# Optimization experiments

Hardware: AMD Instinct MI355X
Metric: run time of the kernel (lower is better)

Reference implementation:

```python
import jax, jax.numpy as jnp
import numpy as np
import math

B, S, HID = 2, 2048, 1024
NH = 16
HD = HID // NH          # 64
VD = HD // 2            # 32 value dim
TD = HD - VD            # 32 type dim
EPS = 1e-6


def setup_inputs() -> dict:
    key = jax.random.key(0)
    ks = jax.random.split(key, 12)
    std = 1.0 / math.sqrt(HID)
    xav = math.sqrt(6.0 / (TD + TD))
    return {
        "x": jax.random.normal(ks[0], (B, S, HID), dtype=jnp.float32),
        "q_w": jax.random.uniform(ks[1], (HID, HID), jnp.float32, -std, std),
        "q_b": jax.random.uniform(ks[2], (HID,), jnp.float32, -std, std),
        "k_w": jax.random.uniform(ks[3], (HID, HID), jnp.float32, -std, std),
        "k_b": jax.random.uniform(ks[4], (HID,), jnp.float32, -std, std),
        "v_w": jax.random.uniform(ks[5], (HID, HID), jnp.float32, -std, std),
        "v_b": jax.random.uniform(ks[6], (HID,), jnp.float32, -std, std),
        "out_w": jax.random.uniform(ks[7], (HID, HID), jnp.float32, -std, std),
        "out_b": jax.random.uniform(ks[8], (HID,), jnp.float32, -std, std),
        "type_bilinear": jax.random.uniform(ks[9], (NH, TD, TD), jnp.float32, -xav, xav),
        "type_bias": jnp.full((NH,), 2.0, dtype=jnp.float32),
        "mask": jnp.ones((B, S), dtype=jnp.int32),
    }


def reference(x, q_w, q_b, k_w, k_b, v_w, v_b, out_w, out_b, type_bilinear, type_bias, mask):
    # projections: [B,S,HID] -> [B,NH,S,HD]
    def proj(w, b):
        y = jnp.einsum("bsi,io->bso", x, w) + b
        return y.reshape(B, S, NH, HD).transpose(0, 2, 1, 3)

    q = proj(q_w, q_b)
    k = proj(k_w, k_b)
    v = proj(v_w, v_b)

    q_val, q_type = q[..., :VD], q[..., VD:]
    k_val, k_type = k[..., :VD], k[..., VD:]

    # standard value score: [B,NH,S,S]
    val_scores = jnp.einsum("bhqd,bhkd->bhqk", q_val, k_val) / math.sqrt(VD)

    # per-head bilinear type score: q_type @ W_h @ k_type^T + bias_h
    qt = jnp.einsum("bhqd,hde->bhqe", q_type, type_bilinear)
    type_scores = jnp.einsum("bhqe,bhke->bhqk", qt, k_type) + type_bias[None, :, None, None]
    type_unif = jax.nn.sigmoid(type_scores)

    scores = val_scores + jnp.log(type_unif + EPS)

    # mask: [B,S] -> broadcast over heads and query dim (keys masked)
    m = (mask[:, None, None, :] != 0)
    scores = jnp.where(m, scores, -jnp.inf)

    attn = jax.nn.softmax(scores, axis=-1)
    out = jnp.einsum("bhqk,bhkd->bhqd", attn, v)          # [B,NH,S,HD]
    out = out.transpose(0, 2, 1, 3).reshape(B, S, HID)
    return jnp.einsum("bsi,io->bso", out, out_w) + out_b
```

## Files before the change

kernel.cpp:

```cpp
#include <hip/hip_runtime.h>
#include <hip/hip_bf16.h>
#include <math.h>

typedef __attribute__((ext_vector_type(8))) short bf16x8;
typedef __attribute__((ext_vector_type(4))) short bf16x4;
typedef __attribute__((ext_vector_type(4))) float f32x4;
typedef __attribute__((ext_vector_type(4))) int   i32x4;

#define NHh 16
#define Sq  2048
#define HIDq 1024
#define HDq 64
#define LOG2E 1.4426950408889634f

#if __has_builtin(__builtin_amdgcn_exp2f)
#define EXP2F(x) __builtin_amdgcn_exp2f(x)
#else
#define EXP2F(x) exp2f(x)
#endif
#if __has_builtin(__builtin_amdgcn_rcpf)
#define RCPF(x) __builtin_amdgcn_rcpf(x)
#else
#define RCPF(x) (1.0f/(x))
#endif

#if __has_builtin(__builtin_amdgcn_mfma_f32_16x16x16bf16_1k)
__device__ __forceinline__ f32x4 MFMA16(bf16x4 a, bf16x4 b, f32x4 c){
  return __builtin_amdgcn_mfma_f32_16x16x16bf16_1k(a, b, c, 0, 0, 0);
}
#else
__device__ __forceinline__ f32x4 MFMA16(bf16x4 a, bf16x4 b, f32x4 c){
  asm volatile("v_mfma_f32_16x16x16_bf16 %0, %1, %2, %0\n\ts_nop 7\n\ts_nop 7"
               : "+v"(c) : "v"(a), "v"(b));
  return c;
}
#endif

__device__ __forceinline__ unsigned short f2bf(float f){
  union { float f; unsigned u; } v; v.f = f;
  unsigned r = v.u + 0x7fffu + ((v.u >> 16) & 1u);
  return (unsigned short)(r >> 16);
}
__device__ __forceinline__ float bf2f(unsigned short s){
  union { unsigned u; float f; } v; v.u = ((unsigned)s) << 16;
  return v.f;
}
__device__ __forceinline__ unsigned pk2bf(float lo, float hi){
  union { __hip_bfloat162 h; unsigned u; } w;
  w.h = __float22bfloat162_rn(make_float2(lo, hi));
  return w.u;
}

__device__ __forceinline__ void gload_lds16(const unsigned short* g, unsigned short* l){
  __builtin_amdgcn_global_load_lds(
      (const __attribute__((address_space(1))) unsigned int*)g,
      (__attribute__((address_space(3))) unsigned int*)l, 16, 0, 0);
}

__global__ __launch_bounds__(256) void prep(const float* __restrict__ x,
                                            unsigned short* __restrict__ xbf,
                                            const int* __restrict__ mask,
                                            unsigned short* __restrict__ Mbf,
                                            const float* __restrict__ w0, const float* __restrict__ w1,
                                            const float* __restrict__ w2, const float* __restrict__ w3,
                                            unsigned short* __restrict__ wT){
  int bid = blockIdx.x;
  int t = threadIdx.x;
  if (bid < 2048){
    int i = bid*256 + t;
    const f32x4* p = (const f32x4*)(x + (size_t)i*8);
    f32x4 a = p[0], b = p[1];
    union { unsigned short us[8]; i32x4 v; } o;
    #pragma unroll
    for (int j=0;j<4;j++){ o.us[j] = f2bf(a[j]); o.us[4+j] = f2bf(b[j]); }
    *(i32x4*)(xbf + (size_t)i*8) = o.v;
  } else if (bid < 2050){
    int base = (bid - 2048)*2048 + t*8;
    #pragma unroll
    for (int j=0;j<8;j++) Mbf[base+j] = mask[base+j] ? (unsigned short)0x3F80 : (unsigned short)0;
  } else {
    __shared__ float tile[32][33];
    int bid2 = bid - 2050;
    int z = bid2 >> 10, rem = bid2 & 1023;
    int bx = rem & 31, by = rem >> 5;
    const float* w = (z==0)?w0:(z==1)?w1:(z==2)?w2:w3;
    unsigned short* dst = wT + (size_t)z*HIDq*HIDq;
    int tx = t & 31, ty = t >> 5;
    int n0 = bx*32, k0 = by*32;
    #pragma unroll
    for (int i=ty;i<32;i+=8) tile[i][tx] = w[(size_t)(k0+i)*HIDq + n0+tx];
    __syncthreads();
    #pragma unroll
    for (int i=ty;i<32;i+=8) dst[(size_t)(n0+i)*HIDq + k0+tx] = f2bf(tile[tx][i]);
  }
}

__device__ __forceinline__ void gemm_core_gl(const unsigned short* __restrict__ Ag,
                                             const unsigned short* __restrict__ Bg,
                                             unsigned short* As, unsigned short* Bs,
                                             int t, int wv, int lane, int wr, int wc, int lr, int g,
                                             f32x4 acc[4][4]){
  for (int k0=0; k0<HIDq; k0+=64){
    __syncthreads();
    #pragma unroll
    for (int j=0;j<4;j++){
      int flat = (j*4+wv)*64 + lane;
      int row = flat>>3, c = flat&7;
      int srcc = (c ^ (row&7))*8;
      gload_lds16(Ag + (size_t)row*HIDq + k0 + srcc, &As[flat*8]);
      gload_lds16(Bg + (size_t)row*HIDq + k0 + srcc, &Bs[flat*8]);
    }
    __syncthreads();
    #pragma unroll
    for (int ks=0; ks<2; ks++){
      bf16x8 af[4], bfv[4];
      #pragma unroll
      for (int m=0;m<4;m++){
        int rr = wr + m*16 + lr;
        af[m]  = *(bf16x8*)&As[rr*64 + (((ks*4+g) ^ (rr&7))*8)];
      }
      #pragma unroll
      for (int n=0;n<4;n++){
        int rr = wc + n*16 + lr;
        bfv[n] = *(bf16x8*)&Bs[rr*64 + (((ks*4+g) ^ (rr&7))*8)];
      }
      #pragma unroll
      for (int n=0;n<4;n++)
        #pragma unroll
        for (int m=0;m<4;m++)
          acc[n][m] = __builtin_amdgcn_mfma_f32_16x16x32_bf16(bfv[n], af[m], acc[n][m], 0,0,0);
    }
  }
}

__global__ __launch_bounds__(256) void gemm_qkv(const unsigned short* __restrict__ xbf,
    const unsigned short* __restrict__ wT,
    const float* __restrict__ q_b, const float* __restrict__ k_b, const float* __restrict__ v_b,
    const int* __restrict__ mask,
    unsigned short* __restrict__ Qeff, unsigned short* __restrict__ Keff,
    unsigned short* __restrict__ Vt){
  __shared__ unsigned short As[128*64];
  __shared__ unsigned short Bs[128*64];
  const int t = threadIdx.x;
  const int wv = t>>6, lane = t&63, g = lane>>4, lr = lane&15;
  const int wr = (wv>>1)*64, wc = (wv&1)*64;
  f32x4 acc[4][4] = {};
  const int bid = blockIdx.x;
  const int xcd = bid & 7, idx = bid >> 3;
  const int xb = (idx % 3)*8 + xcd;
  const int yb = idx / 3;
  const float VS = 0.25501335f;

  if (xb < 16){
    const int row0 = yb*128, col0 = xb*128;
    gemm_core_gl(xbf + (size_t)row0*HIDq, wT + (size_t)col0*HIDq, As, Bs, t, wv, lane, wr, wc, lr, g, acc);
    #pragma unroll
    for (int n=0;n<4;n++){
      #pragma unroll
      for (int m=0;m<4;m++){
        int row = row0 + wr + m*16 + lr;
        int b_ = row>>11, ss = row&2047;
        int colb = col0 + wc + n*16 + g*4;
        int seg = colb>>10, cw = colb&1023;
        int hh = cw>>6, d = cw&63;
        const float* bp = seg ? k_b : q_b;
        f32x4 bb = *(const f32x4*)&bp[cw];
        float sc = seg ? 1.0f : (d < 32 ? VS : -LOG2E);
        unsigned short* E = seg ? Keff : Qeff;
        float v0 = (acc[n][m][0]+bb[0])*sc, v1 = (acc[n][m][1]+bb[1])*sc;
        float v2 = (acc[n][m][2]+bb[2])*sc, v3 = (acc[n][m][3]+bb[3])*sc;
        union { unsigned u[2]; unsigned long long ll; } W;
        W.u[0] = pk2bf(v0,v1); W.u[1] = pk2bf(v2,v3);
        *(unsigned long long*)&E[(((size_t)b_*NHh+hh)*Sq+ss)*HDq + d] = W.ll;
      }
    }
  } else {
    const int row0 = (xb-16)*128, col0 = yb*128;
    gemm_core_gl(wT + (size_t)2*HIDq*HIDq + (size_t)row0*HIDq, xbf + (size_t)col0*HIDq,
                 As, Bs, t, wv, lane, wr, wc, lr, g, acc);
    #pragma unroll
    for (int n=0;n<4;n++){
      #pragma unroll
      for (int m=0;m<4;m++){
        int chan = row0 + wr + m*16 + lr;
        int hh = chan>>6, d = chan&63;
        float bv = v_b[chan];
        int colb = col0 + wc + n*16 + g*4;
        int b_ = colb>>11, ss = colb&2047;
        i32x4 mk = *(const i32x4*)&mask[(size_t)b_*Sq + ss];
        float m0 = mk[0]?1.f:0.f, m1 = mk[1]?1.f:0.f, m2 = mk[2]?1.f:0.f, m3 = mk[3]?1.f:0.f;
        union { unsigned u[2]; unsigned long long ll; } W;
        W.u[0] = pk2bf((acc[n][m][0]+bv)*m0, (acc[n][m][1]+bv)*m1);
        W.u[1] = pk2bf((acc[n][m][2]+bv)*m2, (acc[n][m][3]+bv)*m3);
        *(unsigned long long*)&Vt[(((size_t)b_*NHh+hh)*HDq + d)*Sq + ss] = W.ll;
      }
    }
  }
}

__global__ __launch_bounds__(256) void gemm_out(const unsigned short* __restrict__ A,
                                                const unsigned short* __restrict__ Bt,
                                                const float* __restrict__ bias,
                                                float* __restrict__ C){
  __shared__ unsigned short As[128*64];
  __shared__ unsigned short Bs[64*64];
  const int t = threadIdx.x;
  const int wv = t>>6, lane = t&63, g = lane>>4, lr = lane&15;
  const int wr = (wv>>1)*64, wc = (wv&1)*32;
  const int row0 = blockIdx.y*128, col0 = blockIdx.x*64;
  f32x4 acc[2][4] = {};
  for (int k0=0; k0<HIDq; k0+=64){
    __syncthreads();
    #pragma unroll
    for (int j=0;j<4;j++){
      int flat = t + j*256;
      int row = flat>>3, c = flat&7;
      int srcc = (c ^ (row&7))*8;
      gload_lds16(A + (size_t)(row0+row)*HIDq + k0 + srcc, &As[flat*8]);
    }
    #pragma unroll
    for (int j=0;j<2;j++){
      int flat = t + j*256;
      int row = flat>>3, c = flat&7;
      int srcc = (c ^ (row&7))*8;
      gload_lds16(Bt + (size_t)(col0+row)*HIDq + k0 + srcc, &Bs[flat*8]);
    }
    __syncthreads();
    #pragma unroll
    for (int ks=0; ks<2; ks++){
      bf16x8 af[4], bfv[2];
      #pragma unroll
      for (int m=0;m<4;m++){
        int rr = wr + m*16 + lr;
        af[m]  = *(bf16x8*)&As[rr*64 + (((ks*4+g) ^ (rr&7))*8)];
      }
      #pragma unroll
      for (int n=0;n<2;n++){
        int rr = wc + n*16 + lr;
        bfv[n] = *(bf16x8*)&Bs[rr*64 + (((ks*4+g) ^ (rr&7))*8)];
      }
      #pragma unroll
      for (int n=0;n<2;n++)
        #pragma unroll
        for (int m=0;m<4;m++)
          acc[n][m] = __builtin_amdgcn_mfma_f32_16x16x32_bf16(bfv[n], af[m], acc[n][m], 0,0,0);
    }
  }
  #pragma unroll
  for (int n=0;n<2;n++){
    #pragma unroll
    for (int m=0;m<4;m++){
      int row = row0 + wr + m*16 + lr;
      int colb = col0 + wc + n*16 + g*4;
      f32x4 bb = *(const f32x4*)&bias[colb];
      f32x4 o = acc[n][m] + bb;
      *(f32x4*)&C[(size_t)row*HIDq + colb] = o;
    }
  }
}

__global__ __launch_bounds__(256,4) void attn_kernel(
    const unsigned short* __restrict__ Qe, const unsigned short* __restrict__ Ke,
    const unsigned short* __restrict__ Vt, const float* __restrict__ Tb,
    const float* __restrict__ tbias, const unsigned short* __restrict__ Mbf,
    unsigned short* __restrict__ Obuf)
{
  __shared__ __align__(16) unsigned char smem[40960];
  unsigned short* Kb0 = (unsigned short*)smem;
  unsigned short* Kb1 = (unsigned short*)(smem + 8192);
  unsigned short* Kb2 = (unsigned short*)(smem + 16384);
  unsigned short* Vb0 = (unsigned short*)(smem + 24576);
  unsigned short* Vb1 = (unsigned short*)(smem + 32768);
  float* qls = (float*)smem;
  unsigned short* qtls = Vb1;

  const int t = threadIdx.x;
  const int dd = blockIdx.x;
  const int slot = dd>>3, xcd = dd&7;
  const int x = slot & 31;
  const int bh = ((slot>>5)<<3) | xcd;
  const int h = bh & 15, b = bh >> 4;
  const int q0 = x*64;
  const int wv = t>>6, lane = t&63, g = lane>>4, lr = lane&15;

  const unsigned short* Qb  = Qe + (((size_t)b*NHh+h)*Sq + q0)*HDq;
  const unsigned short* Kb  = Ke + ((size_t)b*NHh+h)*(size_t)Sq*HDq;
  const unsigned short* Vtb = Vt + ((size_t)b*NHh+h)*(size_t)HDq*Sq;
  const unsigned short* Mbfb = Mbf + (size_t)b*Sq;

  {
    int row = t>>2, c8 = (t&3)*8;
    bf16x8 v = *(const bf16x8*)(Qb + (size_t)row*HDq + 32 + c8);
    #pragma unroll
    for (int j=0;j<8;j++) qls[row*33 + c8 + j] = bf2f((unsigned short)v[j]);
  }
  __syncthreads();
  {
    int row = t&63, e0 = (t>>6)*8;
    const float* Th = Tb + (size_t)h*1024;
    float a[8] = {};
    #pragma unroll 4
    for (int d=0; d<32; d++){
      float qd = qls[row*33 + d];
      const f32x4* tp = (const f32x4*)(Th + d*32 + e0);
      f32x4 t0 = tp[0], t1 = tp[1];
      a[0]+=qd*t0[0]; a[1]+=qd*t0[1]; a[2]+=qd*t0[2]; a[3]+=qd*t0[3];
      a[4]+=qd*t1[0]; a[5]+=qd*t1[1]; a[6]+=qd*t1[2]; a[7]+=qd*t1[3];
    }
    __syncthreads();
    union { unsigned u[2]; unsigned long long ll; } W0, W1;
    W0.u[0]=pk2bf(a[0],a[1]); W0.u[1]=pk2bf(a[2],a[3]);
    W1.u[0]=pk2bf(a[4],a[5]); W1.u[1]=pk2bf(a[6],a[7]);
    *(unsigned long long*)&qtls[row*40 + e0]     = W0.ll;
    *(unsigned long long*)&qtls[row*40 + e0 + 4] = W1.ll;
  }
  bf16x8 qvf = *(const bf16x8*)(Qb + (size_t)(wv*16+lr)*HDq + g*8);
  __syncthreads();
  bf16x8 qtn = *(const bf16x8*)&qtls[(wv*16+lr)*40 + g*8];
  __syncthreads();

  #pragma unroll
  for (int i=0;i<2;i++){
    int c = t + i*256;
    int kr = c>>3, kc = c&7;
    gload_lds16(Kb + (size_t)kr*HDq + ((kc ^ (kr&7))*8), Kb0 + c*8);
    int vd = c>>3, vc = c&7;
    gload_lds16(Vtb + (size_t)vd*Sq + ((vc ^ (vd&7))*8), Vb0 + c*8);
    gload_lds16(Kb + (size_t)(64+kr)*HDq + ((kc ^ (kr&7))*8), Kb1 + c*8);
  }
  __syncthreads();

  const float tbn = -tbias[h]*LOG2E;
  const f32x4 tbc = {tbn,tbn,tbn,tbn};
  const f32x4 zf = {0.f,0.f,0.f,0.f};
  f32x4 oT[4] = {};
  f32x4 lsum = {0.f,0.f,0.f,0.f};

  auto phase = [&](const unsigned short* Kc, const unsigned short* Vc, int key0,
                   bool stK, int keyK, unsigned short* Kn,
                   bool stV, int keyV, unsigned short* Vn, bool vm8){
    if (stK){
      #pragma unroll
      for (int i=0;i<2;i++){
        int c = t + i*256;
        int kr = c>>3, kc = c&7;
        gload_lds16(Kb + (size_t)(keyK+kr)*HDq + ((kc ^ (kr&7))*8), Kn + c*8);
      }
    }
    if (stV){
      #pragma unroll
      for (int i=0;i<2;i++){
        int c = t + i*256;
        int vd = c>>3, vc = c&7;
        gload_lds16(Vtb + (size_t)vd*Sq + keyV + ((vc ^ (vd&7))*8), Vn + c*8);
      }
    }
    if (vm8) asm volatile("s_waitcnt vmcnt(8)" ::: "memory");
    else     asm volatile("s_waitcnt vmcnt(4)" ::: "memory");
    __builtin_amdgcn_sched_barrier(0);
    __builtin_amdgcn_s_barrier();

    f32x4 sv[4], st[4];
    __builtin_amdgcn_s_setprio(1);
    #pragma unroll
    for (int ks=0; ks<4; ks++){
      const unsigned short* kb = Kc + (ks*16+lr)*64;
      bf16x8 kf0 = *(const bf16x8*)(kb + (((g  ) ^ (lr&7))*8));
      bf16x8 kf1 = *(const bf16x8*)(kb + (((4+g) ^ (lr&7))*8));
      sv[ks] = __builtin_amdgcn_mfma_f32_16x16x32_bf16(kf0, qvf, zf, 0,0,0);
      st[ks] = __builtin_amdgcn_mfma_f32_16x16x32_bf16(kf1, qtn, tbc, 0,0,0);
    }
    __builtin_amdgcn_s_setprio(0);
    bf16x4 pa[4];
    #pragma unroll
    for (int ks=0; ks<4; ks++){
      float p0 = EXP2F(sv[ks][0]) * RCPF(1.f + EXP2F(st[ks][0]));
      float p1 = EXP2F(sv[ks][1]) * RCPF(1.f + EXP2F(st[ks][1]));
      float p2 = EXP2F(sv[ks][2]) * RCPF(1.f + EXP2F(st[ks][2]));
      float p3 = EXP2F(sv[ks][3]) * RCPF(1.f + EXP2F(st[ks][3]));
      union { unsigned u[2]; bf16x4 v; } P_;
      P_.u[0] = pk2bf(p0,p1); P_.u[1] = pk2bf(p2,p3);
      pa[ks] = P_.v;
    }
    #pragma unroll
    for (int ks=0; ks<4; ks++){
      bf16x4 mfr = *(const bf16x4*)(Mbfb + key0 + ks*16 + g*4);
      __builtin_amdgcn_s_setprio(1);
      lsum = MFMA16(pa[ks], mfr, lsum);
      #pragma unroll
      for (int db=0; db<4; db++){
        bf16x4 vf = *(const bf16x4*)(Vc + (db*16+lr)*64 + (((2*ks + (g>>1)) ^ (lr&7))*8 + 4*(g&1)));
        oT[db] = MFMA16(pa[ks], vf, oT[db]);
      }
      __builtin_amdgcn_s_setprio(0);
    }
    __builtin_amdgcn_s_barrier();
  };

  for (int j=0; j<5; j++){
    int kt = j*384;
    phase(Kb0, Vb0, kt,      true, kt+128, Kb2,  true, kt+64,  Vb1, true);
    phase(Kb1, Vb1, kt+64,   true, kt+192, Kb0,  true, kt+128, Vb0, true);
    phase(Kb2, Vb0, kt+128,  true, kt+256, Kb1,  true, kt+192, Vb1, true);
    phase(Kb0, Vb1, kt+192,  true, kt+320, Kb2,  true, kt+256, Vb0, true);
    phase(Kb1, Vb0, kt+256,  true, kt+384, Kb0,  true, kt+320, Vb1, true);
    phase(Kb2, Vb1, kt+320,  (kt+448 < Sq), kt+448, Kb1,  true, kt+384, Vb0, true);
  }
  phase(Kb0, Vb0, 1920,  false, 0, Kb0,  true, 1984, Vb1, false);
  phase(Kb1, Vb1, 1984,  false, 0, Kb0,  false, 0, Vb0,  false);

  float linv[4];
  #pragma unroll
  for (int r=0;r<4;r++) linv[r] = (lsum[r] > 0.f) ? RCPF(lsum[r]) : 0.f;
  unsigned short* Ob = Obuf + ((size_t)b*Sq + (q0 + wv*16 + g*4))*HIDq + h*HDq + lr;
  #pragma unroll
  for (int db=0; db<4; db++){
    #pragma unroll
    for (int r=0;r<4;r++)
      Ob[(size_t)r*HIDq + db*16] = f2bf(oT[db][r]*linv[r]);
  }
}

extern "C" void kernel_launch(void* const* d_in, const int* in_sizes, int n_in,
                              void* d_out, int out_size, void* d_ws, size_t ws_size,
                              hipStream_t stream) {
  const float* x     = (const float*)d_in[0];
  const float* q_w   = (const float*)d_in[1];
  const float* q_b   = (const float*)d_in[2];
  const float* k_w   = (const float*)d_in[3];
  const float* k_b   = (const float*)d_in[4];
  const float* v_w   = (const float*)d_in[5];
  const float* v_b   = (const float*)d_in[6];
  const float* out_w = (const float*)d_in[7];
  const float* out_b = (const float*)d_in[8];
  const float* Tb    = (const float*)d_in[9];
  const float* tbias = (const float*)d_in[10];
  const int*   mask  = (const int*)d_in[11];

  const size_t MROWS = 4096;
  unsigned short* xbf  = (unsigned short*)d_ws;
  unsigned short* wT   = xbf  + MROWS*HIDq;
  unsigned short* Qeff = wT   + (size_t)4*HIDq*HIDq;
  unsigned short* Keff = Qeff + MROWS*HIDq;
  unsigned short* Vt   = Keff + MROWS*HIDq;
  unsigned short* Obuf = Vt   + MROWS*HIDq;
  unsigned short* Mbf  = Obuf + MROWS*HIDq;

  prep<<<dim3(6146), dim3(256), 0, stream>>>(x, xbf, mask, Mbf, q_w, k_w, v_w, out_w, wT);

  gemm_qkv<<<dim3(768), dim3(256), 0, stream>>>(xbf, wT, q_b, k_b, v_b, mask, Qeff, Keff, Vt);

  attn_kernel<<<dim3(1024), dim3(256), 0, stream>>>(Qeff, Keff, Vt, Tb, tbias, Mbf, Obuf);

  gemm_out<<<dim3(16,32), dim3(256), 0, stream>>>(Obuf, wT + (size_t)3*HIDq*HIDq, out_b, (float*)d_out);
}
```

Before: 149.0 us.

## Fold per-head type bilinear matrix into Q projection weights and bias

A new small kernel multiplies the type half of each head's Q weight columns and bias by that head's bilinear matrix. It overwrites the transposed bf16 Q weights and writes an effective Q bias. The QKV GEMM therefore emits q_type already multiplied by W_h, so the attention kernel drops its per-block prologue (LDS staging, a 32x32 matmul per row, extra barriers) and loads the type fragment straight from global memory. The cost is an extra launch of a 16-block kernel that runs serially after prep and may take a noticeable share of the runtime. Rounding also changes slightly because the folded product is rounded to bf16 in the weights rather than computed per activation.

```diff
diff --git a/kernel.cpp b/kernel.cpp
--- a/kernel.cpp
+++ b/kernel.cpp
@@ -95,6 +95,44 @@
   }
 }
 
+__global__ __launch_bounds__(256) void fold_T(const float* __restrict__ q_w,
+                                              const float* __restrict__ q_b,
+                                              const float* __restrict__ Tb,
+                                              unsigned short* __restrict__ wTq,
+                                              float* __restrict__ qb_eff){
+  __shared__ float Ts[32][33];
+  const int h = blockIdx.x;
+  const int t = threadIdx.x;
+  if (t < 128){
+    int d = t>>2, e0 = (t&3)*8;
+    #pragma unroll
+    for (int j=0;j<8;j++) Ts[d][e0+j] = Tb[h*1024 + d*32 + e0 + j];
+  }
+  __syncthreads();
+  const int col0 = h*64 + 32;
+  if (t < 32){
+    float a = 0.f;
+    #pragma unroll 8
+    for (int d=0; d<32; d++) a += q_b[col0+d]*Ts[d][t];
+    qb_eff[col0 + t] = a;
+  } else if (t < 64){
+    qb_eff[h*64 + (t-32)] = q_b[h*64 + (t-32)];
+  }
+  for (int k = t; k < HIDq; k += 256){
+    float qr[32];
+    const float* src = q_w + (size_t)k*HIDq + col0;
+    #pragma unroll 8
+    for (int d=0;d<32;d++) qr[d] = src[d];
+    #pragma unroll 4
+    for (int e=0;e<32;e++){
+      float a = 0.f;
+      #pragma unroll 8
+      for (int d=0;d<32;d++) a += qr[d]*Ts[d][e];
+      wTq[(size_t)(col0+e)*HIDq + k] = f2bf(a);
+    }
+  }
+}
+
 __device__ __forceinline__ void gemm_core_gl(const unsigned short* __restrict__ Ag,
                                              const unsigned short* __restrict__ Bg,
                                              unsigned short* As, unsigned short* Bs,
@@ -135,7 +173,7 @@
 
 __global__ __launch_bounds__(256) void gemm_qkv(const unsigned short* __restrict__ xbf,
     const unsigned short* __restrict__ wT,
-    const float* __restrict__ q_b, const float* __restrict__ k_b, const float* __restrict__ v_b,
+    const float* __restrict__ qb_eff, const float* __restrict__ k_b, const float* __restrict__ v_b,
     const int* __restrict__ mask,
     unsigned short* __restrict__ Qeff, unsigned short* __restrict__ Keff,
     unsigned short* __restrict__ Vt){
@@ -163,7 +201,7 @@
         int colb = col0 + wc + n*16 + g*4;
         int seg = colb>>10, cw = colb&1023;
         int hh = cw>>6, d = cw&63;
-        const float* bp = seg ? k_b : q_b;
+        const float* bp = seg ? k_b : qb_eff;
         f32x4 bb = *(const f32x4*)&bp[cw];
         float sc = seg ? 1.0f : (d < 32 ? VS : -LOG2E);
         unsigned short* E = seg ? Keff : Qeff;
@@ -261,7 +299,7 @@
 
 __global__ __launch_bounds__(256,4) void attn_kernel(
     const unsigned short* __restrict__ Qe, const unsigned short* __restrict__ Ke,
-    const unsigned short* __restrict__ Vt, const float* __restrict__ Tb,
+    const unsigned short* __restrict__ Vt,
     const float* __restrict__ tbias, const unsigned short* __restrict__ Mbf,
     unsigned short* __restrict__ Obuf)
 {
@@ -271,8 +309,6 @@
   unsigned short* Kb2 = (unsigned short*)(smem + 16384);
   unsigned short* Vb0 = (unsigned short*)(smem + 24576);
   unsigned short* Vb1 = (unsigned short*)(smem + 32768);
-  float* qls = (float*)smem;
-  unsigned short* qtls = Vb1;
 
   const int t = threadIdx.x;
   const int dd = blockIdx.x;
@@ -288,36 +324,8 @@
   const unsigned short* Vtb = Vt + ((size_t)b*NHh+h)*(size_t)HDq*Sq;
   const unsigned short* Mbfb = Mbf + (size_t)b*Sq;
 
-  {
-    int row = t>>2, c8 = (t&3)*8;
-    bf16x8 v = *(const bf16x8*)(Qb + (size_t)row*HDq + 32 + c8);
-    #pragma unroll
-    for (int j=0;j<8;j++) qls[row*33 + c8 + j] = bf2f((unsigned short)v[j]);
-  }
-  __syncthreads();
-  {
-    int row = t&63, e0 = (t>>6)*8;
-    const float* Th = Tb + (size_t)h*1024;
-    float a[8] = {};
-    #pragma unroll 4
-    for (int d=0; d<32; d++){
-      float qd = qls[row*33 + d];
-      const f32x4* tp = (const f32x4*)(Th + d*32 + e0);
-      f32x4 t0 = tp[0], t1 = tp[1];
-      a[0]+=qd*t0[0]; a[1]+=qd*t0[1]; a[2]+=qd*t0[2]; a[3]+=qd*t0[3];
-      a[4]+=qd*t1[0]; a[5]+=qd*t1[1]; a[6]+=qd*t1[2]; a[7]+=qd*t1[3];
-    }
-    __syncthreads();
-    union { unsigned u[2]; unsigned long long ll; } W0, W1;
-    W0.u[0]=pk2bf(a[0],a[1]); W0.u[1]=pk2bf(a[2],a[3]);
-    W1.u[0]=pk2bf(a[4],a[5]); W1.u[1]=pk2bf(a[6],a[7]);
-    *(unsigned long long*)&qtls[row*40 + e0]     = W0.ll;
-    *(unsigned long long*)&qtls[row*40 + e0 + 4] = W1.ll;
-  }
   bf16x8 qvf = *(const bf16x8*)(Qb + (size_t)(wv*16+lr)*HDq + g*8);
-  __syncthreads();
-  bf16x8 qtn = *(const bf16x8*)&qtls[(wv*16+lr)*40 + g*8];
-  __syncthreads();
+  bf16x8 qtn = *(const bf16x8*)(Qb + (size_t)(wv*16+lr)*HDq + 32 + g*8);
 
   #pragma unroll
   for (int i=0;i<2;i++){
@@ -445,12 +453,14 @@
   unsigned short* Vt   = Keff + MROWS*HIDq;
   unsigned short* Obuf = Vt   + MROWS*HIDq;
   unsigned short* Mbf  = Obuf + MROWS*HIDq;
+  float*          qb_eff = (float*)(Mbf + 4096);
 
   prep<<<dim3(6146), dim3(256), 0, stream>>>(x, xbf, mask, Mbf, q_w, k_w, v_w, out_w, wT);
-
-  gemm_qkv<<<dim3(768), dim3(256), 0, stream>>>(xbf, wT, q_b, k_b, v_b, mask, Qeff, Keff, Vt);
-
-  attn_kernel<<<dim3(1024), dim3(256), 0, stream>>>(Qeff, Keff, Vt, Tb, tbias, Mbf, Obuf);
+  fold_T<<<dim3(16), dim3(256), 0, stream>>>(q_w, q_b, Tb, wT, qb_eff);
+
+  gemm_qkv<<<dim3(768), dim3(256), 0, stream>>>(xbf, wT, qb_eff, k_b, v_b, mask, Qeff, Keff, Vt);
+
+  attn_kernel<<<dim3(1024), dim3(256), 0, stream>>>(Qeff, Keff, Vt, tbias, Mbf, Obuf);
 
   gemm_out<<<dim3(16,32), dim3(256), 0, stream>>>(Obuf, wT + (size_t)3*HIDq*HIDq, out_b, (float*)d_out);
 }
```

Measured after the change: 212.3 us. 42.5% more time.
